# Performance work log

Hardware: AMD Instinct MI355X
Metric: run time of the kernel (lower is better)

Reference implementation:

```python
import jax, jax.numpy as jnp
import numpy as np


def setup_inputs() -> dict:
    key = jax.random.key(0)
    k1, k2, k3 = jax.random.split(key, 3)
    B, S, D = 2, 2048, 1024
    N_COMPRESS, RANK = 64, 64
    x = jax.random.normal(k1, (B, S, D), dtype=jnp.float32)
    router_w = jax.random.normal(k2, (N_COMPRESS, D), dtype=jnp.float32) * (1.0 / np.sqrt(D))
    # compress neurons (orthogonal-init in torch; gaussian scaled is fine for a numeric baseline)
    neurons = jax.random.normal(k3, (N_COMPRESS, D, RANK), dtype=jnp.float32) * (1.0 / np.sqrt(D))
    return {"x": x, "router_w": router_w, "neurons": neurons}


TOP_K = 2


def reference(x, router_w, neurons):
    # x: [B,S,D], router_w: [N,D], neurons: [N,D,R]
    B, S, D = x.shape
    R = neurons.shape[-1]
    scores = jnp.einsum('bsd,nd->bsn', x, router_w)            # [B,S,N]
    topk_scores, topk_idx = jax.lax.top_k(scores, TOP_K)       # [B,S,K]
    topk_weights = jax.nn.softmax(topk_scores, axis=-1)        # [B,S,K]
    output = jnp.zeros((B, S, R), dtype=x.dtype)
    for i in range(TOP_K):  # small fixed loop, mirrors original slot-wise combine
        idx = topk_idx[:, :, i]                                # [B,S]
        sel = neurons[idx]                                     # [B,S,D,R] gather
        proj = jnp.einsum('bsd,bsdr->bsr', x, sel)             # per-token matvec
        output = output + topk_weights[:, :, i:i + 1] * proj
    return output, topk_idx, topk_weights
```

## Files before the change

### kernel.cpp

```cpp
#include <hip/hip_runtime.h>
#include <hip/hip_bf16.h>


typedef unsigned short u16;
typedef unsigned int u32;
typedef __attribute__((ext_vector_type(8))) short short8;
typedef __attribute__((ext_vector_type(4))) float f32x4;

__device__ __forceinline__ float bf2f(u16 u) {
    u32 v = ((u32)u) << 16; float f; __builtin_memcpy(&f, &v, 4); return f;
}
__device__ __forceinline__ u16 f2bf(float f) {
    u32 u; __builtin_memcpy(&u, &f, 4);
    u32 r = u + 0x7fff + ((u >> 16) & 1);
    return (u16)(r >> 16);
}
__device__ __forceinline__ u32 pack2(float a, float b) {
    return ((u32)f2bf(b) << 16) | (u32)f2bf(a);
}

#define T_TOKENS 4096
#define DDIM 1024
#define NEXP 64
#define RDIM 64
#define LCAP 1024
#define OUT_IDX_OFF 262144
#define OUT_W_OFF 270336

struct LdBF {
    const u16* p;
    __device__ __forceinline__ float4 ld4(size_t i) const {
        ushort4 v = *(const ushort4*)(p + i);
        return make_float4(bf2f(v.x), bf2f(v.y), bf2f(v.z), bf2f(v.w));
    }
    __device__ __forceinline__ float ld1(size_t i) const { return bf2f(p[i]); }
};
struct LdF32 {
    const float* p;
    __device__ __forceinline__ float4 ld4(size_t i) const { return *(const float4*)(p + i); }
    __device__ __forceinline__ float ld1(size_t i) const { return p[i]; }
};

__device__ __forceinline__ int detect_f32(const u16* x, int* lds_cnt) {
    if (threadIdx.x == 0) *lds_cnt = 0;
    __syncthreads();
    if (threadIdx.x < 256) {
        unsigned e = (x[threadIdx.x] >> 7) & 0xFF;
        if (e >= 0x68 && e <= 0x88) atomicAdd(lds_cnt, 1);
    }
    __syncthreads();
    int f = (*lds_cnt < 200) ? 1 : 0;
    __syncthreads();
    return f;
}

template <class LD>
__device__ __forceinline__ void score_body(LD xld, LD rwld,
                                           float* xs , float* wt ,
                                           float* sc ,
                                           float* out, float* wsW,
                                           int* wsCnt, int* wsList) {
    const int tid = threadIdx.x;
    const size_t t0 = (size_t)blockIdx.x * 8;
    const int wv = tid >> 6;
    const int lane = tid & 63;
    const int tg = lane & 1;
    const int eg = (lane >> 1) & 7;
    const int kql = (lane >> 4) & 3;
    const int dd = 4 * kql + 16 * wv;
    const int kc0 = blockIdx.x & 15;

    if (tid < 128) {
        float4 z = make_float4(0.f, 0.f, 0.f, 0.f);
        ((float4*)out)[(size_t)blockIdx.x * 128 + tid] = z;
    }

    const int sm = tid >> 4;
    const int sd4 = (tid & 15) * 4;

    float acc[4][8];
#pragma unroll
    for (int mi = 0; mi < 4; ++mi)
#pragma unroll
        for (int ei = 0; ei < 8; ++ei) acc[mi][ei] = 0.f;

    float4 px;
    if (tid < 128) px = xld.ld4((t0 + sm) * DDIM + kc0 * 64 + sd4);
    float4 pw[4];
#pragma unroll
    for (int h = 0; h < 4; ++h) {
        int i4 = tid + h * 256;
        pw[h] = rwld.ld4((size_t)(i4 >> 4) * DDIM + kc0 * 64 + (i4 & 15) * 4);
    }

    for (int i = 0; i < 16; ++i) {
        if (i > 0) __syncthreads();
        if (tid < 128) *(float4*)&xs[sm * 68 + sd4] = px;
#pragma unroll
        for (int h = 0; h < 4; ++h) {
            int i4 = tid + h * 256;
            *(float4*)&wt[(i4 >> 4) * 68 + (i4 & 15) * 4] = pw[h];
        }
        __syncthreads();

        if (i < 15) {
            int kn = ((i + 1 + kc0) & 15) * 64;
            if (tid < 128) px = xld.ld4((t0 + sm) * DDIM + kn + sd4);
#pragma unroll
            for (int h = 0; h < 4; ++h) {
                int i4 = tid + h * 256;
                pw[h] = rwld.ld4((size_t)(i4 >> 4) * DDIM + kn + (i4 & 15) * 4);
            }
        }

        float4 xv[4], wv4[8];
#pragma unroll
        for (int mi = 0; mi < 4; ++mi)
            xv[mi] = *(const float4*)&xs[(tg + 2 * mi) * 68 + dd];
#pragma unroll
        for (int ei = 0; ei < 8; ++ei)
            wv4[ei] = *(const float4*)&wt[(eg + 8 * ei) * 68 + dd];
#pragma unroll
        for (int mi = 0; mi < 4; ++mi)
#pragma unroll
            for (int ei = 0; ei < 8; ++ei)
                acc[mi][ei] += xv[mi].x * wv4[ei].x + xv[mi].y * wv4[ei].y +
                               xv[mi].z * wv4[ei].z + xv[mi].w * wv4[ei].w;
    }

#pragma unroll
    for (int mi = 0; mi < 4; ++mi)
#pragma unroll
        for (int ei = 0; ei < 8; ++ei) {
            float v = acc[mi][ei];
            v += __shfl_xor(v, 16, 64);
            v += __shfl_xor(v, 32, 64);
            acc[mi][ei] = v;
        }
    __syncthreads();

    for (int w = 0; w < 4; ++w) {
        if (wv == w && kql == 0) {
#pragma unroll
            for (int mi = 0; mi < 4; ++mi)
#pragma unroll
                for (int ei = 0; ei < 8; ++ei) {
                    int idx = (tg + 2 * mi) * 65 + eg + 8 * ei;
                    sc[idx] = (w == 0) ? acc[mi][ei] : sc[idx] + acc[mi][ei];
                }
        }
        __syncthreads();
    }

    if (tid < 8) {
        const float* s = &sc[tid * 65];
        float best = -1e30f, secv = -1e30f;
        int bi = 0, si = 0;
        for (int j = 0; j < NEXP; ++j) {
            float v = s[j];
            if (v > best) { secv = best; si = bi; best = v; bi = j; }
            else if (v > secv) { secv = v; si = j; }
        }
        float w0 = 1.0f / (1.0f + expf(secv - best));
        float w1 = 1.0f - w0;
        size_t t = t0 + tid;
        out[OUT_IDX_OFF + t * 2 + 0] = (float)bi;
        out[OUT_IDX_OFF + t * 2 + 1] = (float)si;
        out[OUT_W_OFF + t * 2 + 0] = w0;
        out[OUT_W_OFF + t * 2 + 1] = w1;
        wsW[t * 2 + 0] = w0;
        wsW[t * 2 + 1] = w1;
        int p0 = atomicAdd(&wsCnt[bi], 1);
        if (p0 < LCAP) wsList[bi * LCAP + p0] = (int)(t * 2 + 0);
        int p1 = atomicAdd(&wsCnt[si], 1);
        if (p1 < LCAP) wsList[si * LCAP + p1] = (int)(t * 2 + 1);
    }
}

__global__ __launch_bounds__(256, 2) void score_topk(const void* x, const void* rw,
                                                     float* out, float* wsW,
                                                     int* wsCnt, int* wsList) {
    __shared__ float xs[8 * 68];
    __shared__ float wt[64 * 68];
    __shared__ float sc[8 * 65];
    __shared__ int dc;
    int f = detect_f32((const u16*)x, &dc);
    if (f)
        score_body(LdF32{(const float*)x}, LdF32{(const float*)rw}, xs, wt, sc, out, wsW, wsCnt, wsList);
    else
        score_body(LdBF{(const u16*)x}, LdBF{(const u16*)rw}, xs, wt, sc, out, wsW, wsCnt, wsList);
}

template <class LD>
__device__ __forceinline__ void egemm_body(LD xld, LD nld,
                                           const int* wsCnt, const int* wsList,
                                           const float* wsW, float* out,
                                           u16* Ab , u16* Bb ,
                                           int* entL ) {
    const int tid = threadIdx.x;
    const int e = blockIdx.x >> 1;
    const int kh = blockIdx.x & 1;
    const int cntE = min(wsCnt[e], LCAP);
    if (cntE <= 0) return;
    const int wv = tid >> 6;
    const int lane = tid & 63;
    const int l15 = lane & 15, quad = lane >> 4;
    const size_t nbase = (size_t)e * (DDIM * RDIM);

    const int rq = tid & 15;
    const int kpB = tid >> 4;
    for (int s = 0; s < 4; ++s) {
        u32* bb = (u32*)Bb + s * (64 * 68);
        const int k0c = kh * 512 + s * 128;
#pragma unroll
        for (int h = 0; h < 4; ++h) {
            int kp = kpB + h * 16;
            float4 g0 = nld.ld4(nbase + (size_t)(k0c + 2 * kp) * RDIM + rq * 4);
            float4 g1 = nld.ld4(nbase + (size_t)(k0c + 2 * kp + 1) * RDIM + rq * 4);
            bb[(rq * 4 + 0) * 68 + kp] = pack2(g0.x, g1.x);
            bb[(rq * 4 + 1) * 68 + kp] = pack2(g0.y, g1.y);
            bb[(rq * 4 + 2) * 68 + kp] = pack2(g0.z, g1.z);
            bb[(rq * 4 + 3) * 68 + kp] = pack2(g0.w, g1.w);
        }
    }

    const int rowA = tid >> 4;
    const int kqA = tid & 15;

    for (int ti = 0; ti * 16 < cntE; ++ti) {
        const int base = ti * 16;
        const int valid = min(16, cntE - base);
        __syncthreads();
        if (tid < 16)
            entL[tid] = wsList[e * LCAP + base + min(tid, valid - 1)];
        __syncthreads();
        const size_t xrow = (size_t)(entL[rowA] >> 1) * DDIM + kh * 512;

        float4 a0[4], a1[4];
#pragma unroll
        for (int kc = 0; kc < 4; ++kc) {
            a0[kc] = xld.ld4(xrow + kc * 128 + kqA * 8);
            a1[kc] = xld.ld4(xrow + kc * 128 + kqA * 8 + 4);
        }
#pragma unroll
        for (int kc = 0; kc < 4; ++kc) {
            uint4 w;
            w.x = pack2(a0[kc].x, a0[kc].y);
            w.y = pack2(a0[kc].z, a0[kc].w);
            w.z = pack2(a1[kc].x, a1[kc].y);
            w.w = pack2(a1[kc].z, a1[kc].w);
            *(uint4*)&((u32*)Ab)[kc * (16 * 68) + rowA * 68 + kqA * 4] = w;
        }
        __syncthreads();

        f32x4 acc = {0.f, 0.f, 0.f, 0.f};
#pragma unroll
        for (int kc = 0; kc < 4; ++kc)
#pragma unroll
            for (int ko = 0; ko < 4; ++ko) {
                int kofs = ko * 32 + quad * 8;
                short8 bfr = *(const short8*)&Bb[kc * (64 * 136) + (16 * wv + l15) * 136 + kofs];
                short8 af = *(const short8*)&Ab[kc * (16 * 136) + l15 * 136 + kofs];
                acc = __builtin_amdgcn_mfma_f32_16x16x32_bf16(af, bfr, acc, 0, 0, 0);
            }

#pragma unroll
        for (int reg = 0; reg < 4; ++reg) {
            int m = quad * 4 + reg;
            if (m < valid) {
                int t2 = entL[m];
                atomicAdd(&out[(size_t)(t2 >> 1) * RDIM + 16 * wv + l15], wsW[t2] * acc[reg]);
            }
        }
    }
}

__global__ __launch_bounds__(256, 1) void expert_gemm(const void* x, const void* neurons,
                                                      const int* wsCnt, const int* wsList,
                                                      const float* wsW, float* out) {
    __shared__ u16 Ab[4 * 16 * 136];
    __shared__ u16 Bb[4 * 64 * 136];
    __shared__ int entL[16];
    __shared__ int dc;
    int f = detect_f32((const u16*)x, &dc);
    if (f)
        egemm_body(LdF32{(const float*)x}, LdF32{(const float*)neurons}, wsCnt, wsList, wsW, out, Ab, Bb, entL);
    else
        egemm_body(LdBF{(const u16*)x}, LdBF{(const u16*)neurons}, wsCnt, wsList, wsW, out, Ab, Bb, entL);
}

extern "C" void kernel_launch(void* const* d_in, const int* in_sizes, int n_in,
                              void* d_out, int out_size, void* d_ws, size_t ws_size,
                              hipStream_t stream) {
    const void* x = d_in[0];
    const void* rw = d_in[1];
    const void* neurons = d_in[2];
    float* out = (float*)d_out;

    char* wsc = (char*)d_ws;
    float* wsW = (float*)wsc;
    int* wsCnt = (int*)(wsc + 32 * 1024);
    int* wsList = (int*)((char*)wsCnt + 256);

    hipMemsetAsync(wsCnt, 0, 256, stream);
    score_topk<<<512, 256, 0, stream>>>(x, rw, out, wsW, wsCnt, wsList);
    expert_gemm<<<128, 256, 0, stream>>>(x, neurons, wsCnt, wsList, wsW, out);
}
```

Measured before the change: 145.9 us.

## Split expert GEMM across 8 K-slices and replace atomics with partial buffer plus combine

The expert GEMM grid grows from 128 blocks (2 K-halves per expert) to 512 blocks (8 K-slices of 128 per expert), which cuts per-block shared memory and allows 2 blocks per CU. Each block writes its partial projections into a workspace buffer P instead of doing weighted atomicAdd into the output. A new combine kernel sums the 8 partials for each slot and applies the top-k weights, so zeroing the output in the score kernel is no longer needed. Within the GEMM loop, the next tile's x rows are prefetched into registers before the current tile's MFMAs are issued. The costs are an extra kernel launch and extra global traffic for P, in exchange for more parallelism and no atomic contention.

```diff
diff --git a/kernel.cpp b/kernel.cpp
--- a/kernel.cpp
+++ b/kernel.cpp
@@ -70,11 +70,6 @@
     const int dd = 4 * kql + 16 * wv;
     const int kc0 = blockIdx.x & 15;
 
-    if (tid < 128) {
-        float4 z = make_float4(0.f, 0.f, 0.f, 0.f);
-        ((float4*)out)[(size_t)blockIdx.x * 128 + tid] = z;
-    }
-
     const int sm = tid >> 4;
     const int sd4 = (tid & 15) * 4;
 
@@ -194,99 +189,118 @@
 template <class LD>
 __device__ __forceinline__ void egemm_body(LD xld, LD nld,
                                            const int* wsCnt, const int* wsList,
-                                           const float* wsW, float* out,
+                                           float* P,
                                            u16* Ab , u16* Bb ,
-                                           int* entL ) {
+                                           int* eL ) {
     const int tid = threadIdx.x;
-    const int e = blockIdx.x >> 1;
-    const int kh = blockIdx.x & 1;
+    const int e = blockIdx.x >> 3;
+    const int oct = blockIdx.x & 7;
     const int cntE = min(wsCnt[e], LCAP);
     if (cntE <= 0) return;
     const int wv = tid >> 6;
     const int lane = tid & 63;
     const int l15 = lane & 15, quad = lane >> 4;
     const size_t nbase = (size_t)e * (DDIM * RDIM);
-
-    const int rq = tid & 15;
-    const int kpB = tid >> 4;
-    for (int s = 0; s < 4; ++s) {
-        u32* bb = (u32*)Bb + s * (64 * 68);
-        const int k0c = kh * 512 + s * 128;
+    const int k0 = oct * 128;
+
+    for (int j = tid; j < cntE; j += 256) eL[j] = wsList[e * LCAP + j];
+
+    {
+        const int rq = tid & 15;
+        const int kpB = tid >> 4;
+        u32* bb = (u32*)Bb;
 #pragma unroll
         for (int h = 0; h < 4; ++h) {
             int kp = kpB + h * 16;
-            float4 g0 = nld.ld4(nbase + (size_t)(k0c + 2 * kp) * RDIM + rq * 4);
-            float4 g1 = nld.ld4(nbase + (size_t)(k0c + 2 * kp + 1) * RDIM + rq * 4);
+            float4 g0 = nld.ld4(nbase + (size_t)(k0 + 2 * kp) * RDIM + rq * 4);
+            float4 g1 = nld.ld4(nbase + (size_t)(k0 + 2 * kp + 1) * RDIM + rq * 4);
             bb[(rq * 4 + 0) * 68 + kp] = pack2(g0.x, g1.x);
             bb[(rq * 4 + 1) * 68 + kp] = pack2(g0.y, g1.y);
             bb[(rq * 4 + 2) * 68 + kp] = pack2(g0.z, g1.z);
             bb[(rq * 4 + 3) * 68 + kp] = pack2(g0.w, g1.w);
         }
     }
+    __syncthreads();
 
     const int rowA = tid >> 4;
     const int kqA = tid & 15;
-
-    for (int ti = 0; ti * 16 < cntE; ++ti) {
+    const int ntiles = (cntE + 15) >> 4;
+
+    float4 a0, a1;
+    {
+        int t2r = eL[min(rowA, cntE - 1)];
+        size_t xrow = (size_t)(t2r >> 1) * DDIM + k0;
+        a0 = xld.ld4(xrow + kqA * 8);
+        a1 = xld.ld4(xrow + kqA * 8 + 4);
+    }
+
+    for (int ti = 0; ti < ntiles; ++ti) {
         const int base = ti * 16;
         const int valid = min(16, cntE - base);
+        if (ti > 0) __syncthreads();
+        {
+            uint4 w;
+            w.x = pack2(a0.x, a0.y);
+            w.y = pack2(a0.z, a0.w);
+            w.z = pack2(a1.x, a1.y);
+            w.w = pack2(a1.z, a1.w);
+            *(uint4*)&((u32*)Ab)[rowA * 68 + kqA * 4] = w;
+        }
         __syncthreads();
-        if (tid < 16)
-            entL[tid] = wsList[e * LCAP + base + min(tid, valid - 1)];
-        __syncthreads();
-        const size_t xrow = (size_t)(entL[rowA] >> 1) * DDIM + kh * 512;
-
-        float4 a0[4], a1[4];
-#pragma unroll
-        for (int kc = 0; kc < 4; ++kc) {
-            a0[kc] = xld.ld4(xrow + kc * 128 + kqA * 8);
-            a1[kc] = xld.ld4(xrow + kc * 128 + kqA * 8 + 4);
-        }
-#pragma unroll
-        for (int kc = 0; kc < 4; ++kc) {
-            uint4 w;
-            w.x = pack2(a0[kc].x, a0[kc].y);
-            w.y = pack2(a0[kc].z, a0[kc].w);
-            w.z = pack2(a1[kc].x, a1[kc].y);
-            w.w = pack2(a1[kc].z, a1[kc].w);
-            *(uint4*)&((u32*)Ab)[kc * (16 * 68) + rowA * 68 + kqA * 4] = w;
-        }
-        __syncthreads();
+        if (ti + 1 < ntiles) {
+            int t2r = eL[min(base + 16 + rowA, cntE - 1)];
+            size_t xrow = (size_t)(t2r >> 1) * DDIM + k0;
+            a0 = xld.ld4(xrow + kqA * 8);
+            a1 = xld.ld4(xrow + kqA * 8 + 4);
+        }
 
         f32x4 acc = {0.f, 0.f, 0.f, 0.f};
 #pragma unroll
-        for (int kc = 0; kc < 4; ++kc)
-#pragma unroll
-            for (int ko = 0; ko < 4; ++ko) {
-                int kofs = ko * 32 + quad * 8;
-                short8 bfr = *(const short8*)&Bb[kc * (64 * 136) + (16 * wv + l15) * 136 + kofs];
-                short8 af = *(const short8*)&Ab[kc * (16 * 136) + l15 * 136 + kofs];
-                acc = __builtin_amdgcn_mfma_f32_16x16x32_bf16(af, bfr, acc, 0, 0, 0);
-            }
+        for (int ko = 0; ko < 4; ++ko) {
+            int kofs = ko * 32 + quad * 8;
+            short8 bfr = *(const short8*)&Bb[(16 * wv + l15) * 136 + kofs];
+            short8 af = *(const short8*)&Ab[l15 * 136 + kofs];
+            acc = __builtin_amdgcn_mfma_f32_16x16x32_bf16(af, bfr, acc, 0, 0, 0);
+        }
 
 #pragma unroll
         for (int reg = 0; reg < 4; ++reg) {
             int m = quad * 4 + reg;
             if (m < valid) {
-                int t2 = entL[m];
-                atomicAdd(&out[(size_t)(t2 >> 1) * RDIM + 16 * wv + l15], wsW[t2] * acc[reg]);
+                int t2 = eL[base + m];
+                P[(size_t)t2 * 512 + oct * 64 + 16 * wv + l15] = acc[reg];
             }
         }
     }
 }
 
-__global__ __launch_bounds__(256, 1) void expert_gemm(const void* x, const void* neurons,
+__global__ __launch_bounds__(256, 2) void expert_gemm(const void* x, const void* neurons,
                                                       const int* wsCnt, const int* wsList,
-                                                      const float* wsW, float* out) {
-    __shared__ u16 Ab[4 * 16 * 136];
-    __shared__ u16 Bb[4 * 64 * 136];
-    __shared__ int entL[16];
+                                                      float* P) {
+    __shared__ u16 Ab[16 * 136];
+    __shared__ u16 Bb[64 * 136];
+    __shared__ int eL[LCAP];
     __shared__ int dc;
     int f = detect_f32((const u16*)x, &dc);
     if (f)
-        egemm_body(LdF32{(const float*)x}, LdF32{(const float*)neurons}, wsCnt, wsList, wsW, out, Ab, Bb, entL);
+        egemm_body(LdF32{(const float*)x}, LdF32{(const float*)neurons}, wsCnt, wsList, P, Ab, Bb, eL);
     else
-        egemm_body(LdBF{(const u16*)x}, LdBF{(const u16*)neurons}, wsCnt, wsList, wsW, out, Ab, Bb, entL);
+        egemm_body(LdBF{(const u16*)x}, LdBF{(const u16*)neurons}, wsCnt, wsList, P, Ab, Bb, eL);
+}
+
+__global__ __launch_bounds__(256) void combine(const float* P, const float* wsW,
+                                               float* out) {
+    int i = blockIdx.x * 256 + threadIdx.x;
+    int t = i >> 6, r = i & 63;
+    const float* p0 = P + (size_t)(2 * t) * 512 + r;
+    const float* p1 = P + (size_t)(2 * t + 1) * 512 + r;
+    float s0 = 0.f, s1 = 0.f;
+#pragma unroll
+    for (int o = 0; o < 8; ++o) {
+        s0 += p0[o * 64];
+        s1 += p1[o * 64];
+    }
+    out[i] = wsW[2 * t] * s0 + wsW[2 * t + 1] * s1;
 }
 
 extern "C" void kernel_launch(void* const* d_in, const int* in_sizes, int n_in,
@@ -301,8 +315,10 @@
     float* wsW = (float*)wsc;
     int* wsCnt = (int*)(wsc + 32 * 1024);
     int* wsList = (int*)((char*)wsCnt + 256);
+    float* P = (float*)(wsc + (1 << 20));
 
     hipMemsetAsync(wsCnt, 0, 256, stream);
     score_topk<<<512, 256, 0, stream>>>(x, rw, out, wsW, wsCnt, wsList);
-    expert_gemm<<<128, 256, 0, stream>>>(x, neurons, wsCnt, wsList, wsW, out);
-}
+    expert_gemm<<<512, 256, 0, stream>>>(x, neurons, wsCnt, wsList, P);
+    combine<<<1024, 256, 0, stream>>>(P, wsW, out);
+}
```

Result: faster. 126.1 us (-13.6%).
